# Kernel optimization log

Measured on AMD Instinct MI355X. Metric: run time of the kernel, lower is better.

Reference implementation:

```python
import jax, jax.numpy as jnp
import numpy as np

M, D, A, H = 16384, 256, 264, 8
HD = A // H  # 33
B = 512
THRESH = 0.1
DECAY = 0.95


def setup_inputs() -> dict:
    key = jax.random.key(0)
    ks = jax.random.split(key, 16)
    rn = lambda i, shape, scale=1.0: jax.random.normal(ks[i], shape, dtype=jnp.float32) * scale
    return {
        "features": rn(0, (B, D)),
        "gradients": rn(1, (B, D), 0.1),
        "mem_keys": rn(2, (M, D)),
        "mem_values": rn(3, (M, D)),
        "mem_ages": jax.random.uniform(ks[4], (M,), dtype=jnp.float32, minval=0.0, maxval=50.0),
        "mem_surprise": jax.random.uniform(ks[5], (M,), dtype=jnp.float32, minval=0.0, maxval=5.0),
        "Wk": rn(6, (D, D), 1.0 / np.sqrt(D)), "bk": jnp.zeros((D,), jnp.float32),
        "Wv": rn(7, (D, D), 1.0 / np.sqrt(D)), "bv": jnp.zeros((D,), jnp.float32),
        "Wp": rn(8, (D, A), 1.0 / np.sqrt(D)), "bp": jnp.zeros((A,), jnp.float32),
        "Win": rn(9, (A, 3 * A), 1.0 / np.sqrt(A)), "b_in": jnp.zeros((3 * A,), jnp.float32),
        "Wout": rn(10, (A, A), 1.0 / np.sqrt(A)), "bout": jnp.zeros((A,), jnp.float32),
        "Wo": rn(11, (A, D), 1.0 / np.sqrt(A)), "bo": jnp.zeros((D,), jnp.float32),
    }


def reference(features, gradients, mem_keys, mem_values, mem_ages, mem_surprise,
              Wk, bk, Wv, bv, Wp, bp, Win, b_in, Wout, bout, Wo, bo):
    # ---- compute_surprise: grad norm * min cdist to memory keys ----
    d2 = (jnp.sum(features * features, 1)[:, None]
          + jnp.sum(mem_keys * mem_keys, 1)[None, :]
          - 2.0 * features @ mem_keys.T)                      # [B, M]
    min_dist = jnp.sqrt(jnp.clip(jnp.min(d2, axis=1), 0.0))   # [B]
    surprise = jnp.linalg.norm(gradients, axis=-1) * min_dist  # [B]
    memorize = surprise > THRESH                               # [B] bool

    # ---- write_memory: sequential per-item eviction (argmin of decayed surprise) ----
    def step(carry, xs):
        mk, mv, ages, surp = carry
        feat, s_i, w = xs
        slot = jnp.argmin(surp * DECAY ** ages)
        mk = mk.at[slot].set(jnp.where(w, feat @ Wk + bk, mk[slot]))
        mv = mv.at[slot].set(jnp.where(w, feat @ Wv + bv, mv[slot]))
        ages = ages.at[slot].set(jnp.where(w, 0.0, ages[slot]))
        surp = surp.at[slot].set(jnp.where(w, s_i, surp[slot]))
        return (mk, mv, ages, surp), None

    (mem_keys, mem_values, mem_ages, mem_surprise), _ = jax.lax.scan(
        step, (mem_keys, mem_values, mem_ages, mem_surprise),
        (features, surprise, memorize))

    # ---- read_memory: project, 8-head cross attention (1 query vs M slots) ----
    q = features @ Wp + bp        # [B, A]
    kf = mem_keys @ Wp + bp       # [M, A]
    vf = mem_values @ Wp + bp     # [M, A]
    Wq_, Wk_, Wv_ = jnp.split(Win, 3, axis=1)
    bq_, bk_, bv_ = jnp.split(b_in, 3)
    qh = (q @ Wq_ + bq_).reshape(B, H, HD)
    kh = (kf @ Wk_ + bk_).reshape(M, H, HD)
    vh = (vf @ Wv_ + bv_).reshape(M, H, HD)
    scores = jnp.einsum('bhd,mhd->bhm', qh, kh) / np.float32(np.sqrt(HD))
    attn = jax.nn.softmax(scores, axis=-1)                    # [B, H, M]
    ctx = jnp.einsum('bhm,mhd->bhd', attn, vh).reshape(B, A)
    retrieved = (ctx @ Wout + bout) @ Wo + bo                 # [B, D]
    return retrieved
```

## Files before the change

kernel.cpp:

```cpp
#include <hip/hip_runtime.h>
#include <math.h>

typedef unsigned short ushort_t;
typedef float v4f __attribute__((ext_vector_type(4)));
typedef short v8s __attribute__((ext_vector_type(8)));

#define ATTN_MS 16

__device__ __forceinline__ unsigned fenc(float f){
  unsigned b = __float_as_uint(f);
  return (b & 0x80000000u) ? ~b : (b | 0x80000000u);
}
__device__ __forceinline__ float fdec(unsigned u){
  unsigned b = (u & 0x80000000u) ? (u ^ 0x80000000u) : ~u;
  return __uint_as_float(b);
}
__device__ __forceinline__ ushort_t bf16_rne(float x){
  unsigned u = __float_as_uint(x);
  unsigned r = u + 0x7FFFu + ((u >> 16) & 1u);
  return (ushort_t)(r >> 16);
}
__device__ __forceinline__ void split2(float x, ushort_t& h, ushort_t& l){
  unsigned u = __float_as_uint(x);
  unsigned r = u + 0x7FFFu + ((u >> 16) & 1u);
  h = (ushort_t)(r >> 16);
  float hf = __uint_as_float(r & 0xFFFF0000u);
  l = bf16_rne(x - hf);
}
__device__ __forceinline__ float bf2f(ushort_t x){ return __uint_as_float(((unsigned)x) << 16); }
union U8 { v8s v; ushort_t u[8]; };

__global__ __launch_bounds__(256) void prep_all(
    const float* __restrict__ features, const float* __restrict__ gradients,
    const float* __restrict__ mem_keys, const float* __restrict__ mem_values,
    ushort_t* __restrict__ FH, ushort_t* __restrict__ FL,
    ushort_t* __restrict__ MKH, ushort_t* __restrict__ MKL,
    ushort_t* __restrict__ MVH, ushort_t* __restrict__ MVL,
    float* __restrict__ k2, float* __restrict__ f2, float* __restrict__ gn,
    unsigned* __restrict__ minD2, ushort_t* __restrict__ VtGH, ushort_t* __restrict__ VtGL){
  int y = blockIdx.y, bx = blockIdx.x, t = threadIdx.x;
  if (y == 3){
    if (bx >= 3840) return;
    const int PER4 = 8*15*16384/4;
    int idx = bx*256 + t;
    if (idx >= 2*PER4) return;
    ushort_t* base = (idx < PER4) ? VtGH : VtGL;
    int i = (idx < PER4) ? idx : idx - PER4;
    int s = i*4;
    int hh = s / (15*16384);
    int r2 = s - hh*(15*16384);
    int row = 33 + (r2 >> 14);
    int col = r2 & 16383;
    ushort4 z; z.x = 0; z.y = 0; z.z = 0; z.w = 0;
    *(ushort4*)(base + (size_t)(hh*48 + row)*16384 + col) = z;
    return;
  }
  int wid = t >> 6, lane = t & 63;
  int row = bx*4 + wid;
  if (y == 2 && bx >= 128) return;
  const float* src = (y == 0) ? mem_keys : (y == 1) ? mem_values : features;
  float4 v = *(const float4*)(src + (size_t)row*256 + lane*4);
  ushort_t h0,h1,h2,h3,l0,l1,l2,l3;
  split2(v.x,h0,l0); split2(v.y,h1,l1); split2(v.z,h2,l2); split2(v.w,h3,l3);
  uint2 hp = make_uint2((unsigned)h0 | ((unsigned)h1<<16), (unsigned)h2 | ((unsigned)h3<<16));
  uint2 lp = make_uint2((unsigned)l0 | ((unsigned)l1<<16), (unsigned)l2 | ((unsigned)l3<<16));
  ushort_t* H = (y == 0) ? MKH : (y == 1) ? MVH : FH;
  ushort_t* L = (y == 0) ? MKL : (y == 1) ? MVL : FL;
  *(uint2*)(H + (size_t)row*256 + lane*4) = hp;
  *(uint2*)(L + (size_t)row*256 + lane*4) = lp;
  if (y == 1) return;
  float s = v.x*v.x + v.y*v.y + v.z*v.z + v.w*v.w;
  if (y == 0){
    for (int off = 32; off > 0; off >>= 1) s += __shfl_down(s, off, 64);
    if (lane == 0) k2[row] = s;
  } else {
    float4 g = *(const float4*)(gradients + (size_t)row*256 + lane*4);
    float tg = g.x*g.x + g.y*g.y + g.z*g.z + g.w*g.w;
    for (int off = 32; off > 0; off >>= 1){ s += __shfl_down(s, off, 64); tg += __shfl_down(tg, off, 64); }
    if (lane == 0){ f2[row] = s; gn[row] = sqrtf(tg); minD2[row] = 0xFFFFFFFFu; }
  }
}

__global__ __launch_bounds__(256) void gemm_bias(const float* __restrict__ A, const float* __restrict__ W,
                                                 const float* __restrict__ bias, float* __restrict__ C,
                                                 const float* __restrict__ W2, const float* __restrict__ bias2,
                                                 float* __restrict__ C2,
                                                 int M, int K, int N, int ldw, int woff){
  if (blockIdx.z == 1){ W = W2; bias = bias2; C = C2; }
  __shared__ float As[32*68];
  __shared__ float Ws[32*68];
  int m0 = blockIdx.x*64, c0 = blockIdx.y*64;
  int t = threadIdx.x;
  int mq = (t & 15)*4, cq = (t >> 4)*4;
  float acc[16];
  #pragma unroll
  for (int i = 0; i < 16; ++i) acc[i] = 0.f;
  for (int k0 = 0; k0 < K; k0 += 32){
    #pragma unroll
    for (int i = 0; i < 2; ++i){
      int idx = t + 256*i;
      int row = idx >> 3, kk = (idx & 7)*4;
      int gm = m0 + row, gk = k0 + kk;
      float x=0.f, y=0.f, z=0.f, w=0.f;
      if (gm < M){
        const float* ap = A + (size_t)gm*K + gk;
        if (gk + 3 < K){ float4 v = *(const float4*)ap; x=v.x; y=v.y; z=v.z; w=v.w; }
        else {
          if (gk   < K) x = ap[0];
          if (gk+1 < K) y = ap[1];
          if (gk+2 < K) z = ap[2];
          if (gk+3 < K) w = ap[3];
        }
      }
      As[(kk+0)*68+row]=x; As[(kk+1)*68+row]=y; As[(kk+2)*68+row]=z; As[(kk+3)*68+row]=w;
    }
    #pragma unroll
    for (int i = 0; i < 2; ++i){
      int idx = t + 256*i;
      int kk = idx >> 4, cc = (idx & 15)*4;
      int gk = k0 + kk, gc = c0 + cc;
      float4 v = make_float4(0.f,0.f,0.f,0.f);
      if (gk < K){
        const float* wp = W + (size_t)gk*ldw + woff + gc;
        if (gc + 3 < N) v = *(const float4*)wp;
        else {
          if (gc   < N) v.x = wp[0];
          if (gc+1 < N) v.y = wp[1];
          if (gc+2 < N) v.z = wp[2];
          if (gc+3 < N) v.w = wp[3];
        }
      }
      *(float4*)(Ws + kk*68 + cc) = v;
    }
    __syncthreads();
    #pragma unroll
    for (int j = 0; j < 32; ++j){
      float4 a = *(const float4*)(As + j*68 + mq);
      float4 w = *(const float4*)(Ws + j*68 + cq);
      acc[ 0]+=a.x*w.x; acc[ 1]+=a.x*w.y; acc[ 2]+=a.x*w.z; acc[ 3]+=a.x*w.w;
      acc[ 4]+=a.y*w.x; acc[ 5]+=a.y*w.y; acc[ 6]+=a.y*w.z; acc[ 7]+=a.y*w.w;
      acc[ 8]+=a.z*w.x; acc[ 9]+=a.z*w.y; acc[10]+=a.z*w.z; acc[11]+=a.z*w.w;
      acc[12]+=a.w*w.x; acc[13]+=a.w*w.y; acc[14]+=a.w*w.z; acc[15]+=a.w*w.w;
    }
    __syncthreads();
  }
  #pragma unroll
  for (int i = 0; i < 4; ++i){
    int gm = m0 + mq + i;
    if (gm >= M) continue;
    #pragma unroll
    for (int j = 0; j < 4; ++j){
      int gc = c0 + cq + j;
      if (gc >= N) continue;
      C[(size_t)gm*N + gc] = acc[i*4+j] + (bias ? bias[gc] : 0.f);
    }
  }
}

__global__ __launch_bounds__(256) void wprep_gemm(
    const float* __restrict__ Wp, const float* __restrict__ Win,
    const float* __restrict__ Wout, const float* __restrict__ Wo,
    const float* __restrict__ bp, const float* __restrict__ b_in,
    const float* __restrict__ bout, const float* __restrict__ bo,
    ushort_t* __restrict__ WtkH, ushort_t* __restrict__ WtkL,
    ushort_t* __restrict__ WtvH, ushort_t* __restrict__ WtvL,
    ushort_t* __restrict__ WtqH, ushort_t* __restrict__ WtqL,
    float* __restrict__ Wpk, float* __restrict__ Wpv, float* __restrict__ Wco,
    float* __restrict__ bpq, float* __restrict__ bpk, float* __restrict__ bpv, float* __restrict__ bco){
  __shared__ float As[32*68];
  __shared__ float Ws[32*68];
  int z = blockIdx.z;
  int t = threadIdx.x;
  if (z == 4){
    int flat = (blockIdx.x*5 + blockIdx.y)*256 + t;
    if (flat < 264){
      float a = b_in[flat];
      for (int k = 0; k < 264; ++k) a += bp[k]*Win[(size_t)k*792 + flat];
      bpq[flat] = a;
    } else if (flat < 528){
      int c = flat - 264;
      float a = b_in[264 + c];
      for (int k = 0; k < 264; ++k) a += bp[k]*Win[(size_t)k*792 + 264 + c];
      bpk[c] = a;
    } else if (flat < 792){
      int c = flat - 528;
      float a = b_in[528 + c];
      for (int k = 0; k < 264; ++k) a += bp[k]*Win[(size_t)k*792 + 528 + c];
      bpv[c] = a;
    } else if (flat < 1048){
      int c = flat - 792;
      float a = bo[c];
      for (int k = 0; k < 264; ++k) a += bout[k]*Wo[(size_t)k*256 + c];
      bco[c] = a;
    }
    return;
  }
  const float* A = (z < 3) ? Wp : Wout;
  const float* W = (z < 3) ? Win : Wo;
  const int M = (z < 3) ? 256 : 264;
  const int K = 264;
  const int N = (z < 3) ? 264 : 256;
  const int ldw = (z < 3) ? 792 : 256;
  const int woff = (z == 0) ? 264 : (z == 1) ? 528 : 0;
  int m0 = blockIdx.x*64, c0 = blockIdx.y*64;
  int mq = (t & 15)*4, cq = (t >> 4)*4;
  float acc[16];
  #pragma unroll
  for (int i = 0; i < 16; ++i) acc[i] = 0.f;
  for (int k0 = 0; k0 < K; k0 += 32){
    #pragma unroll
    for (int i = 0; i < 2; ++i){
      int idx = t + 256*i;
      int row = idx >> 3, kk = (idx & 7)*4;
      int gm = m0 + row, gk = k0 + kk;
      float x=0.f, y=0.f, z2=0.f, w=0.f;
      if (gm < M){
        const float* ap = A + (size_t)gm*K + gk;
        if (gk + 3 < K){ float4 v = *(const float4*)ap; x=v.x; y=v.y; z2=v.z; w=v.w; }
        else {
          if (gk   < K) x = ap[0];
          if (gk+1 < K) y = ap[1];
          if (gk+2 < K) z2 = ap[2];
          if (gk+3 < K) w = ap[3];
        }
      }
      As[(kk+0)*68+row]=x; As[(kk+1)*68+row]=y; As[(kk+2)*68+row]=z2; As[(kk+3)*68+row]=w;
    }
    #pragma unroll
    for (int i = 0; i < 2; ++i){
      int idx = t + 256*i;
      int kk = idx >> 4, cc = (idx & 15)*4;
      int gk = k0 + kk, gc = c0 + cc;
      float4 v = make_float4(0.f,0.f,0.f,0.f);
      if (gk < K){
        const float* wp = W + (size_t)gk*ldw + woff + gc;
        if (gc + 3 < N) v = *(const float4*)wp;
        else {
          if (gc   < N) v.x = wp[0];
          if (gc+1 < N) v.y = wp[1];
          if (gc+2 < N) v.z = wp[2];
          if (gc+3 < N) v.w = wp[3];
        }
      }
      *(float4*)(Ws + kk*68 + cc) = v;
    }
    __syncthreads();
    #pragma unroll
    for (int j = 0; j < 32; ++j){
      float4 a = *(const float4*)(As + j*68 + mq);
      float4 w = *(const float4*)(Ws + j*68 + cq);
      acc[ 0]+=a.x*w.x; acc[ 1]+=a.x*w.y; acc[ 2]+=a.x*w.z; acc[ 3]+=a.x*w.w;
      acc[ 4]+=a.y*w.x; acc[ 5]+=a.y*w.y; acc[ 6]+=a.y*w.z; acc[ 7]+=a.y*w.w;
      acc[ 8]+=a.z*w.x; acc[ 9]+=a.z*w.y; acc[10]+=a.z*w.z; acc[11]+=a.z*w.w;
      acc[12]+=a.w*w.x; acc[13]+=a.w*w.y; acc[14]+=a.w*w.z; acc[15]+=a.w*w.w;
    }
    __syncthreads();
  }
  if (z < 3){
    ushort_t* WH = (z==0) ? WtkH : (z==1) ? WtvH : WtqH;
    ushort_t* WL = (z==0) ? WtkL : (z==1) ? WtvL : WtqL;
    float* Wf = (z==0) ? Wpk : (z==1) ? Wpv : nullptr;
    #pragma unroll
    for (int i = 0; i < 4; ++i){
      int gm = m0 + mq + i;
      if (gm >= 256) continue;
      #pragma unroll
      for (int j = 0; j < 4; ++j){
        int gc = c0 + cq + j;
        float r = acc[i*4+j];
        ushort_t hh, ll; split2(r, hh, ll);
        WH[(size_t)gc*256 + gm] = hh;
        WL[(size_t)gc*256 + gm] = ll;
        if (Wf && gc < 264) Wf[(size_t)gm*264 + gc] = r;
      }
    }
  } else {
    #pragma unroll
    for (int i = 0; i < 4; ++i){
      int gm = m0 + mq + i;
      if (gm >= 264) continue;
      #pragma unroll
      for (int j = 0; j < 4; ++j){
        int gc = c0 + cq + j;
        if (gc < 256) Wco[(size_t)gm*256 + gc] = acc[i*4+j];
      }
    }
  }
}

__global__ __launch_bounds__(256) void big_mfma(
    const ushort_t* __restrict__ FH, const ushort_t* __restrict__ FL,
    const ushort_t* __restrict__ MKH, const ushort_t* __restrict__ MKL,
    const ushort_t* __restrict__ MVH, const ushort_t* __restrict__ MVL,
    const ushort_t* __restrict__ WtqH, const ushort_t* __restrict__ WtqL,
    const ushort_t* __restrict__ WtkH, const ushort_t* __restrict__ WtkL,
    const ushort_t* __restrict__ WtvH, const ushort_t* __restrict__ WtvL,
    const float* __restrict__ bpq, const float* __restrict__ bpk, const float* __restrict__ bpv,
    const float* __restrict__ k2,
    float* __restrict__ qh, ushort_t* __restrict__ khH, ushort_t* __restrict__ khL,
    ushort_t* __restrict__ VtGH, ushort_t* __restrict__ VtGL, unsigned* __restrict__ minD2){
  int z = blockIdx.z;
  int bx = blockIdx.x, by = blockIdx.y;
  if (z == 0 && bx >= 4) return;
  if (z != 3 && by >= 5) return;
  __shared__ ushort_t AsH[128*40];
  __shared__ ushort_t AsL[128*40];
  __shared__ ushort_t BsH[64*40];
  __shared__ ushort_t BsL[64*40];
  __shared__ unsigned sminU[64];
  const ushort_t* AH = (z == 0) ? FH : (z == 2) ? MVH : MKH;
  const ushort_t* AL = (z == 0) ? FL : (z == 2) ? MVL : MKL;
  const ushort_t* BH = (z == 0) ? WtqH : (z == 1) ? WtkH : (z == 2) ? WtvH : FH;
  const ushort_t* BL = (z == 0) ? WtqL : (z == 1) ? WtkL : WtvL;
  const float* bias = (z == 0) ? bpq : (z == 1) ? bpk : bpv;
  int t = threadIdx.x;
  int m0 = bx*128, n0 = by*64;
  int lane = t & 63, w = t >> 6;
  int wm = (w & 1)*64, wn = (w >> 1)*32;
  int l15 = lane & 15, q = lane >> 4;
  if (z == 3 && t < 64) sminU[t] = 0xFFFFFFFFu;
  v4f acc[4][2];
  #pragma unroll
  for (int i = 0; i < 4; ++i)
    #pragma unroll
    for (int j = 0; j < 2; ++j) acc[i][j] = (v4f){0.f,0.f,0.f,0.f};

  for (int k0 = 0; k0 < 256; k0 += 32){
    #pragma unroll
    for (int rdx = 0; rdx < 2; ++rdx){
      int idx = t + 256*rdx;
      int row = idx >> 2, ch = idx & 3;
      *(uint4*)(AsH + row*40 + ch*8) = *(const uint4*)(AH + (size_t)(m0+row)*256 + k0 + ch*8);
      if (z < 3)
        *(uint4*)(AsL + row*40 + ch*8) = *(const uint4*)(AL + (size_t)(m0+row)*256 + k0 + ch*8);
    }
    {
      int row = t >> 2, ch = t & 3;
      *(uint4*)(BsH + row*40 + ch*8) = *(const uint4*)(BH + (size_t)(n0+row)*256 + k0 + ch*8);
      if (z < 3)
        *(uint4*)(BsL + row*40 + ch*8) = *(const uint4*)(BL + (size_t)(n0+row)*256 + k0 + ch*8);
    }
    __syncthreads();
    if (z < 3){
      v8s aH[4], aL[4], bH[2], bL[2];
      #pragma unroll
      for (int im = 0; im < 4; ++im){
        aH[im] = *(const v8s*)(AsH + (wm + im*16 + l15)*40 + q*8);
        aL[im] = *(const v8s*)(AsL + (wm + im*16 + l15)*40 + q*8);
      }
      #pragma unroll
      for (int jn = 0; jn < 2; ++jn){
        bH[jn] = *(const v8s*)(BsH + (wn + jn*16 + l15)*40 + q*8);
        bL[jn] = *(const v8s*)(BsL + (wn + jn*16 + l15)*40 + q*8);
      }
      #pragma unroll
      for (int im = 0; im < 4; ++im)
        #pragma unroll
        for (int jn = 0; jn < 2; ++jn){
          acc[im][jn] = __builtin_amdgcn_mfma_f32_16x16x32_bf16(aH[im], bH[jn], acc[im][jn], 0, 0, 0);
          acc[im][jn] = __builtin_amdgcn_mfma_f32_16x16x32_bf16(aH[im], bL[jn], acc[im][jn], 0, 0, 0);
          acc[im][jn] = __builtin_amdgcn_mfma_f32_16x16x32_bf16(aL[im], bH[jn], acc[im][jn], 0, 0, 0);
        }
    } else {
      v8s aH[4], bH[2];
      #pragma unroll
      for (int im = 0; im < 4; ++im) aH[im] = *(const v8s*)(AsH + (wm + im*16 + l15)*40 + q*8);
      #pragma unroll
      for (int jn = 0; jn < 2; ++jn) bH[jn] = *(const v8s*)(BsH + (wn + jn*16 + l15)*40 + q*8);
      #pragma unroll
      for (int im = 0; im < 4; ++im)
        #pragma unroll
        for (int jn = 0; jn < 2; ++jn)
          acc[im][jn] = __builtin_amdgcn_mfma_f32_16x16x32_bf16(aH[im], bH[jn], acc[im][jn], 0, 0, 0);
    }
    __syncthreads();
  }

  if (z == 3){
    float kk[4][4];
    #pragma unroll
    for (int im = 0; im < 4; ++im)
      #pragma unroll
      for (int r = 0; r < 4; ++r) kk[im][r] = k2[m0 + wm + im*16 + q*4 + r];
    #pragma unroll
    for (int jn = 0; jn < 2; ++jn){
      float mv = INFINITY;
      #pragma unroll
      for (int im = 0; im < 4; ++im)
        #pragma unroll
        for (int r = 0; r < 4; ++r)
          mv = fminf(mv, kk[im][r] - 2.f*acc[im][jn][r]);
      mv = fminf(mv, __shfl_xor(mv, 16, 64));
      mv = fminf(mv, __shfl_xor(mv, 32, 64));
      if (q == 0) atomicMin(&sminU[wn + jn*16 + l15], fenc(mv));
    }
    __syncthreads();
    if (t < 64) atomicMin(&minD2[n0 + t], sminU[t]);
    return;
  }
  #pragma unroll
  for (int im = 0; im < 4; ++im){
    #pragma unroll
    for (int jn = 0; jn < 2; ++jn){
      int n = n0 + wn + jn*16 + l15;
      if (n >= 264) continue;
      float bv = bias[n];
      int mb = m0 + wm + im*16 + q*4;
      if (z == 0){
        #pragma unroll
        for (int r = 0; r < 4; ++r) qh[(size_t)(mb+r)*264 + n] = acc[im][jn][r] + bv;
      } else if (z == 1){
        int hh = n/33, dd = n - hh*33;
        int col = hh*40 + dd;
        #pragma unroll
        for (int r = 0; r < 4; ++r){
          ushort_t sh, sl; split2(acc[im][jn][r] + bv, sh, sl);
          khH[(size_t)(mb+r)*320 + col] = sh;
          khL[(size_t)(mb+r)*320 + col] = sl;
        }
      } else {
        int hh = n/33, dd = n - hh*33;
        size_t rowb = (size_t)(hh*48 + dd)*16384 + mb;
        ushort4 hv, lv;
        split2(acc[im][jn][0] + bv, hv.x, lv.x);
        split2(acc[im][jn][1] + bv, hv.y, lv.y);
        split2(acc[im][jn][2] + bv, hv.z, lv.z);
        split2(acc[im][jn][3] + bv, hv.w, lv.w);
        *(ushort4*)(VtGH + rowb) = hv;
        *(ushort4*)(VtGL + rowb) = lv;
      }
    }
  }
}

#define SCAN_CAP 1024
__global__ __launch_bounds__(1024) void scan_kernel(
    const float* __restrict__ mem_surprise, const float* __restrict__ mem_ages,
    const unsigned* __restrict__ minD2, const float* __restrict__ f2, const float* __restrict__ gn,
    float* __restrict__ parr, int* __restrict__ slotForB, int* __restrict__ lastB){
  __shared__ unsigned hist[2048];
  __shared__ float candV[SCAN_CAP];
  __shared__ int   candI[SCAN_CAP];
  __shared__ float tv[1024];
  __shared__ int   ti[1024];
  __shared__ float ssur[512];
  __shared__ int   smemz[512];
  __shared__ int   wtot[16];
  __shared__ int   sh_misc[8];
  int t = threadIdx.x;

  int mem = 0;
  if (t < 512){
    float d2 = fdec(minD2[t]) + f2[t];
    float s = gn[t]*sqrtf(fmaxf(d2, 0.f));
    ssur[t] = s;
    mem = (s > 0.1f) ? 1 : 0;
    smemz[t] = mem;
  }
  const float LN095 = -0.05129329438755058f;
  #pragma unroll
  for (int j = 0; j < 16; ++j){
    int m = t*16 + j;
    float p = mem_surprise[m] * __expf(mem_ages[m] * LN095);
    parr[m] = p;
    lastB[m] = -1;
  }
  hist[t] = 0u; hist[t + 1024] = 0u;
  if (t < 8) sh_misc[t] = (t == 3) ? 0x7F800000 : 0;
  __syncthreads();
  #pragma unroll
  for (int j = 0; j < 16; ++j){
    int m = t*16 + j;
    unsigned key = __float_as_uint(parr[m]) >> 20;
    if (key > 2047u) key = 2047u;
    atomicAdd(&hist[key], 1u);
  }
  __syncthreads();
  if (t < 512){ ti[t] = (int)(hist[4*t] + hist[4*t+1] + hist[4*t+2] + hist[4*t+3]); }
  __syncthreads();
  if (t < 32){ int s = 0; for (int i = 0; i < 16; ++i) s += ti[16*t + i]; ti[512 + t] = s; }
  __syncthreads();
  if (t == 0){
    int cum = 0, i2 = 0;
    for (; i2 < 32; ++i2){ if (cum + ti[512+i2] >= 512) break; cum += ti[512+i2]; }
    int i1 = i2*16;
    for (;; ++i1){ if (cum + ti[i1] >= 512) break; cum += ti[i1]; }
    int bin = i1*4;
    for (;; ++bin){ if (cum + (int)hist[bin] >= 512) break; cum += (int)hist[bin]; }
    sh_misc[1] = bin;
  }
  __syncthreads();
  int threshKey = sh_misc[1];
  #pragma unroll
  for (int j = 0; j < 16; ++j){
    int m = t*16 + j;
    unsigned key = __float_as_uint(parr[m]) >> 20;
    if (key > 2047u) key = 2047u;
    if ((int)key <= threshKey){
      int pos = atomicAdd(&sh_misc[0], 1);
      if (pos < SCAN_CAP){ candV[pos] = parr[m]; candI[pos] = m; }
    }
  }
  __syncthreads();
  int cnt = sh_misc[0];
  if (t >= cnt && t < SCAN_CAP){ candV[t] = INFINITY; candI[t] = 0x7FFFFFFF; }
  __syncthreads();
  for (int ksz = 2; ksz <= SCAN_CAP; ksz <<= 1){
    for (int jj = ksz >> 1; jj > 0; jj >>= 1){
      int ixj = t ^ jj;
      if (ixj > t){
        float v1 = candV[t], v2 = candV[ixj];
        int i1 = candI[t], i2 = candI[ixj];
        bool lt21 = (v2 < v1) || (v2 == v1 && i2 < i1);
        bool lt12 = (v1 < v2) || (v1 == v2 && i1 < i2);
        bool up = ((t & ksz) == 0);
        bool sw = up ? lt21 : lt12;
        if (sw){ candV[t] = v2; candI[t] = i2; candV[ixj] = v1; candI[ixj] = i1; }
      }
      __syncthreads();
    }
  }
  int lp = 0;
  if (t < 512){
    unsigned long long mask = __ballot(mem != 0);
    int lane = t & 63;
    lp = __popcll(mask & ((1ull << lane) - 1ull));
    if (lane == 0) wtot[t >> 6] = __popcll(mask);
  }
  if (t < 512 && mem) atomicMin(&sh_misc[3], __float_as_int(ssur[t]));
  __syncthreads();
  if (t == 0){
    int ksum = 0;
    for (int wv = 0; wv < 8; ++wv) ksum += wtot[wv];
    sh_misc[4] = ksum;
    bool okf = (cnt <= SCAN_CAP) && (ksum <= cnt);
    if (okf && ksum > 0){
      float minw = __int_as_float(sh_misc[3]);
      okf = (minw > candV[ksum - 1]);
    }
    sh_misc[2] = okf ? 1 : 0;
  }
  __syncthreads();
  if (sh_misc[2] == 1){
    if (t < 512){
      int wv = t >> 6, base = 0;
      for (int i = 0; i < wv; ++i) base += wtot[i];
      int slot = -1;
      if (mem){ slot = candI[base + lp]; atomicMax(&lastB[slot], t); }
      slotForB[t] = slot;
    }
  } else {
    for (int b = 0; b < 512; ++b){
      float bv = parr[t*16]; int bi = t*16;
      #pragma unroll
      for (int j = 1; j < 16; ++j){
        float v = parr[t*16 + j];
        if (v < bv){ bv = v; bi = t*16 + j; }
      }
      tv[t] = bv; ti[t] = bi;
      __syncthreads();
      for (int s = 512; s > 0; s >>= 1){
        if (t < s){
          float v2 = tv[t+s]; int i2 = ti[t+s];
          if (v2 < tv[t] || (v2 == tv[t] && i2 < ti[t])){ tv[t] = v2; ti[t] = i2; }
        }
        __syncthreads();
      }
      int slot = ti[0];
      int memb = smemz[b];
      if (t == 0) slotForB[b] = memb ? slot : -1;
      if (memb && t == (slot >> 4)) parr[slot] = ssur[b];
      __syncthreads();
    }
    if (t < 512){ int s = slotForB[t]; if (s >= 0) atomicMax(&lastB[s], t); }
  }
}

__global__ __launch_bounds__(64) void fixup_rows(const int* __restrict__ slotForB, const int* __restrict__ lastB,
                                                 const float* __restrict__ newK, const float* __restrict__ newV,
                                                 const float* __restrict__ Wpk, const float* __restrict__ Wpv,
                                                 const float* __restrict__ bpk, const float* __restrict__ bpv,
                                                 ushort_t* __restrict__ khH, ushort_t* __restrict__ khL,
                                                 ushort_t* __restrict__ VtH, ushort_t* __restrict__ VtL){
  int b = blockIdx.x;
  int slot = slotForB[b];
  if (slot < 0) return;
  if (lastB[slot] != b) return;
  __shared__ float kr[256], vr[256];
  int t = threadIdx.x;
  *(float4*)(kr + t*4) = *(const float4*)(newK + (size_t)b*256 + t*4);
  *(float4*)(vr + t*4) = *(const float4*)(newV + (size_t)b*256 + t*4);
  __syncthreads();
  for (int c = t; c < 264; c += 64){
    float aK = bpk[c], aV = bpv[c];
    for (int k = 0; k < 256; ++k){
      aK += kr[k]*Wpk[(size_t)k*264 + c];
      aV += vr[k]*Wpv[(size_t)k*264 + c];
    }
    int hh = c/33, dd = c - hh*33;
    ushort_t sh, sl;
    split2(aK, sh, sl);
    khH[(size_t)slot*320 + hh*40 + dd] = sh;
    khL[(size_t)slot*320 + hh*40 + dd] = sl;
    split2(aV, sh, sl);
    VtH[(size_t)(hh*48 + dd)*16384 + slot] = sh;
    VtL[(size_t)(hh*48 + dd)*16384 + slot] = sl;
  }
}

__global__ __launch_bounds__(256, 3) void attn_mfma(
    const float* __restrict__ qh, const ushort_t* __restrict__ khH, const ushort_t* __restrict__ khL,
    const ushort_t* __restrict__ VtGH, const ushort_t* __restrict__ VtGL,
    float* __restrict__ pm, float* __restrict__ pl, float* __restrict__ pctx){
  const int h = blockIdx.x, bt = blockIdx.y, ms = blockIdx.z;
  const int b0 = bt*64, mbase = ms*(16384/ATTN_MS);
  const int t = threadIdx.x, lane = t & 63, w = t >> 6;
  const int l15 = lane & 15, q = lane >> 4;
  __shared__ ushort_t KH[64*40], KL[64*40];
  __shared__ ushort_t VsH[48*72], VsL[48*72];
  __shared__ ushort_t PH[4*16*72], PL[4*16*72];
  __shared__ float k32f[64];
  const float scale = 0.17407765595569785f;

  const int bq = b0 + 16*w + l15;
  U8 qHU, qLU;
  {
    const float* qp = qh + (size_t)bq*264 + h*33 + q*8;
    #pragma unroll
    for (int j = 0; j < 8; ++j) split2(qp[j]*scale, qHU.u[j], qLU.u[j]);
  }
  const v8s bQH = qHU.v, bQL = qLU.v;
  const float q32v = qh[(size_t)bq*264 + h*33 + 32]*scale;
  float rMv = -INFINITY, rLv = 0.f;
  v4f cacc[3];
  #pragma unroll
  for (int i = 0; i < 3; ++i) cacc[i] = (v4f){0.f,0.f,0.f,0.f};
  ushort_t* PHw = PH + w*16*72;
  ushort_t* PLw = PL + w*16*72;

  for (int mt = 0; mt < 16384/ATTN_MS/64; ++mt){
    const int m0 = mbase + mt*64;
    __syncthreads();
    {
      int ml = t >> 2, ch = t & 3;
      *(uint4*)(KH + ml*40 + ch*8) = *(const uint4*)(khH + (size_t)(m0+ml)*320 + h*40 + ch*8);
      *(uint4*)(KL + ml*40 + ch*8) = *(const uint4*)(khL + (size_t)(m0+ml)*320 + h*40 + ch*8);
      if (t < 64)
        k32f[t] = bf2f(khH[(size_t)(m0+t)*320 + h*40 + 32]) + bf2f(khL[(size_t)(m0+t)*320 + h*40 + 32]);
    }
    #pragma unroll
    for (int i = 0; i < 3; ++i){
      int idx = t + 256*i;
      int arr = idx >= 384;
      int rem = idx - arr*384;
      int row = rem >> 3, ch = rem & 7;
      const ushort_t* g = (arr ? VtGL : VtGH) + (size_t)(h*48 + row)*16384 + m0 + ch*8;
      *(uint4*)((arr ? VsL : VsH) + row*72 + ch*8) = *(const uint4*)g;
    }
    __syncthreads();
    v4f s4[4];
    #pragma unroll
    for (int im = 0; im < 4; ++im){
      v8s aH = *(const v8s*)(KH + (im*16 + l15)*40 + q*8);
      v8s aL = *(const v8s*)(KL + (im*16 + l15)*40 + q*8);
      v4f sv = (v4f){0.f,0.f,0.f,0.f};
      sv = __builtin_amdgcn_mfma_f32_16x16x32_bf16(aH, bQH, sv, 0, 0, 0);
      sv = __builtin_amdgcn_mfma_f32_16x16x32_bf16(aH, bQL, sv, 0, 0, 0);
      sv = __builtin_amdgcn_mfma_f32_16x16x32_bf16(aL, bQH, sv, 0, 0, 0);
      s4[im] = sv;
    }
    #pragma unroll
    for (int im = 0; im < 4; ++im)
      #pragma unroll
      for (int r = 0; r < 4; ++r) s4[im][r] += k32f[im*16 + q*4 + r]*q32v;
    float mx = -INFINITY;
    #pragma unroll
    for (int im = 0; im < 4; ++im)
      #pragma unroll
      for (int r = 0; r < 4; ++r) mx = fmaxf(mx, s4[im][r]);
    mx = fmaxf(mx, __shfl_xor(mx, 16, 64));
    mx = fmaxf(mx, __shfl_xor(mx, 32, 64));
    float nm = fmaxf(rMv, mx);
    float alf = __expf(rMv - nm);
    rMv = nm;
    float sm = 0.f;
    #pragma unroll
    for (int im = 0; im < 4; ++im){
      v4f p;
      #pragma unroll
      for (int r = 0; r < 4; ++r){ p[r] = __expf(s4[im][r] - nm); sm += p[r]; }
      ushort4 hv, lv;
      split2(p[0], hv.x, lv.x); split2(p[1], hv.y, lv.y);
      split2(p[2], hv.z, lv.z); split2(p[3], hv.w, lv.w);
      *(ushort4*)(PHw + l15*72 + im*16 + q*4) = hv;
      *(ushort4*)(PLw + l15*72 + im*16 + q*4) = lv;
    }
    sm += __shfl_xor(sm, 16, 64);
    sm += __shfl_xor(sm, 32, 64);
    rLv = rLv*alf + sm;
    #pragma unroll
    for (int r = 0; r < 4; ++r){
      float ar = __shfl(alf, q*4 + r, 64);
      cacc[0][r] *= ar; cacc[1][r] *= ar; cacc[2][r] *= ar;
    }
    #pragma unroll
    for (int ks = 0; ks < 2; ++ks){
      v8s paH = *(const v8s*)(PHw + l15*72 + ks*32 + q*8);
      v8s paL = *(const v8s*)(PLw + l15*72 + ks*32 + q*8);
      #pragma unroll
      for (int tile = 0; tile < 3; ++tile){
        v8s vbH = *(const v8s*)(VsH + (tile*16 + l15)*72 + ks*32 + q*8);
        v8s vbL = *(const v8s*)(VsL + (tile*16 + l15)*72 + ks*32 + q*8);
        cacc[tile] = __builtin_amdgcn_mfma_f32_16x16x32_bf16(paH, vbH, cacc[tile], 0, 0, 0);
        cacc[tile] = __builtin_amdgcn_mfma_f32_16x16x32_bf16(paH, vbL, cacc[tile], 0, 0, 0);
        cacc[tile] = __builtin_amdgcn_mfma_f32_16x16x32_bf16(paL, vbH, cacc[tile], 0, 0, 0);
      }
    }
  }
  int g = (h*8 + bt)*ATTN_MS + ms;
  if (q == 0){
    pm[(size_t)g*64 + 16*w + l15] = rMv;
    pl[(size_t)g*64 + 16*w + l15] = rLv;
  }
  #pragma unroll
  for (int tile = 0; tile < 3; ++tile){
    int d = tile*16 + l15;
    if (d < 33){
      #pragma unroll
      for (int r = 0; r < 4; ++r)
        pctx[((size_t)g*64 + 16*w + q*4 + r)*33 + d] = cacc[tile][r];
    }
  }
}

__global__ __launch_bounds__(256) void combine_kernel(const float* __restrict__ pm, const float* __restrict__ pl,
                                                      const float* __restrict__ pctx, float* __restrict__ ctxf){
  int idx = blockIdx.x*256 + threadIdx.x;
  if (idx >= 512*264) return;
  int b = idx / 264, c = idx - b*264;
  int h = c / 33, d = c - h*33;
  int bt = b >> 6, bl = b & 63;
  int g0 = (h*8 + bt)*ATTN_MS;
  float gm = -INFINITY;
  for (int ms = 0; ms < ATTN_MS; ++ms) gm = fmaxf(gm, pm[(g0+ms)*64 + bl]);
  float L = 0.f, cv = 0.f;
  for (int ms = 0; ms < ATTN_MS; ++ms){
    int gg = (g0+ms)*64 + bl;
    float w = __expf(pm[gg] - gm);
    L += pl[gg]*w;
    cv += pctx[(size_t)gg*33 + d]*w;
  }
  ctxf[idx] = cv / L;
}

extern "C" void kernel_launch(void* const* d_in, const int* in_sizes, int n_in,
                              void* d_out, int out_size, void* d_ws, size_t ws_size,
                              hipStream_t stream){
  (void)in_sizes; (void)n_in; (void)out_size; (void)ws_size;
  const float* features     = (const float*)d_in[0];
  const float* gradients    = (const float*)d_in[1];
  const float* mem_keys     = (const float*)d_in[2];
  const float* mem_values   = (const float*)d_in[3];
  const float* mem_ages     = (const float*)d_in[4];
  const float* mem_surprise = (const float*)d_in[5];
  const float* Wk   = (const float*)d_in[6];
  const float* bk   = (const float*)d_in[7];
  const float* Wv   = (const float*)d_in[8];
  const float* bv   = (const float*)d_in[9];
  const float* Wp   = (const float*)d_in[10];
  const float* bp   = (const float*)d_in[11];
  const float* Win  = (const float*)d_in[12];
  const float* b_in = (const float*)d_in[13];
  const float* Wout = (const float*)d_in[14];
  const float* bout = (const float*)d_in[15];
  const float* Wo   = (const float*)d_in[16];
  const float* bo   = (const float*)d_in[17];
  float* out = (float*)d_out;

  float* w = (float*)d_ws;
  size_t off = 0;
  auto alloc = [&](size_t n)->float*{ float* p = w + off; off += (n + 63) & ~(size_t)63; return p; };
  float*    k2       = alloc(16384);
  unsigned* minD2    = (unsigned*)alloc(512);
  float*    f2       = alloc(512);
  float*    gn       = alloc(512);
  int*      slotForB = (int*)alloc(512);
  int*      lastB    = (int*)alloc(16384);
  float*    parr     = alloc(16384);
  float*    newK     = alloc((size_t)512*256);
  float*    newV     = alloc((size_t)512*256);
  float*    qh       = alloc((size_t)512*264);
  ushort_t* khH      = (ushort_t*)alloc((size_t)16384*320/2);
  ushort_t* khL      = (ushort_t*)alloc((size_t)16384*320/2);
  ushort_t* VtGH     = (ushort_t*)alloc((size_t)8*48*16384/2);
  ushort_t* VtGL     = (ushort_t*)alloc((size_t)8*48*16384/2);
  float*    MKbase   = alloc((size_t)16384*256/2*2);
  ushort_t* MKH      = (ushort_t*)MKbase;
  ushort_t* MKL      = (ushort_t*)(MKbase + (size_t)16384*256/2);
  float*    MVbase   = alloc((size_t)16384*256/2*2);
  ushort_t* MVH      = (ushort_t*)MVbase;
  ushort_t* MVL      = (ushort_t*)(MVbase + (size_t)16384*256/2);
  ushort_t* FH       = (ushort_t*)alloc((size_t)512*256/2);
  ushort_t* FL       = (ushort_t*)alloc((size_t)512*256/2);
  float*    Wpk      = alloc((size_t)256*264);
  float*    Wpv      = alloc((size_t)256*264);
  float*    Wco      = alloc((size_t)264*256);
  ushort_t* WtkH     = (ushort_t*)alloc((size_t)320*256/2);
  ushort_t* WtkL     = (ushort_t*)alloc((size_t)320*256/2);
  ushort_t* WtvH     = (ushort_t*)alloc((size_t)320*256/2);
  ushort_t* WtvL     = (ushort_t*)alloc((size_t)320*256/2);
  ushort_t* WtqH     = (ushort_t*)alloc((size_t)320*256/2);
  ushort_t* WtqL     = (ushort_t*)alloc((size_t)320*256/2);
  float*    bpq      = alloc(264);
  float*    bpk      = alloc(264);
  float*    bpv      = alloc(264);
  float*    bco      = alloc(256);
  float*    pm       = MKbase;
  float*    pl       = MKbase + (size_t)ATTN_MS*64*64;
  float*    ctxf     = pl + (size_t)ATTN_MS*64*64;
  float*    pctx     = MVbase;

  prep_all<<<dim3(4096,4), 256, 0, stream>>>(features, gradients, mem_keys, mem_values,
      FH, FL, MKH, MKL, MVH, MVL, k2, f2, gn, minD2, VtGH, VtGL);

  wprep_gemm<<<dim3(5,5,5), 256, 0, stream>>>(Wp, Win, Wout, Wo, bp, b_in, bout, bo,
      WtkH, WtkL, WtvH, WtvL, WtqH, WtqL, Wpk, Wpv, Wco, bpq, bpk, bpv, bco);

  gemm_bias<<<dim3(8,4,2), 256, 0, stream>>>(features, Wk, bk, newK, Wv, bv, newV, 512, 256, 256, 256, 0);

  big_mfma<<<dim3(128,8,4), 256, 0, stream>>>(FH, FL, MKH, MKL, MVH, MVL,
      WtqH, WtqL, WtkH, WtkL, WtvH, WtvL, bpq, bpk, bpv, k2,
      qh, khH, khL, VtGH, VtGL, minD2);

  scan_kernel<<<1, 1024, 0, stream>>>(mem_surprise, mem_ages, minD2, f2, gn, parr, slotForB, lastB);
  fixup_rows<<<512, 64, 0, stream>>>(slotForB, lastB, newK, newV, Wpk, Wpv, bpk, bpv, khH, khL, VtGH, VtGL);

  attn_mfma<<<dim3(8,8,ATTN_MS), 256, 0, stream>>>(qh, khH, khL, VtGH, VtGL, pm, pl, pctx);
  combine_kernel<<<528, 256, 0, stream>>>(pm, pl, pctx, ctxf);
  gemm_bias<<<dim3(8,4,1), 256, 0, stream>>>(ctxf, Wco, bco, out, Wco, bco, out, 512, 264, 256, 256, 0);
}
```

Before: 427.8 us.

## Stage GEMM and attention tiles via direct global-to-LDS loads with XOR swizzle

Replaces register-staged global-to-shared copies in big_mfma and attn_mfma with global_load_lds 16-byte direct transfers. Padded LDS rows are removed, and the V tile gets an XOR swizzle to avoid bank conflicts. Occupancy hints rise to 4 blocks per CU. The aim is to cut VGPR pressure and load/store instruction overhead. The trade-off is that the unpadded K/A tiles may now hit LDS bank conflicts.

```diff
diff --git a/kernel.cpp b/kernel.cpp
--- a/kernel.cpp
+++ b/kernel.cpp
@@ -1,5 +1,6 @@
 #include <hip/hip_runtime.h>
 #include <math.h>
+#include <stdint.h>
 
 typedef unsigned short ushort_t;
 typedef float v4f __attribute__((ext_vector_type(4)));
@@ -29,6 +30,13 @@
 }
 __device__ __forceinline__ float bf2f(ushort_t x){ return __uint_as_float(((unsigned)x) << 16); }
 union U8 { v8s v; ushort_t u[8]; };
+
+__device__ __forceinline__ void gl2lds16(const void* g, void* l){
+  __builtin_amdgcn_global_load_lds(
+      (const __attribute__((address_space(1))) unsigned int*)(uintptr_t)g,
+      (__attribute__((address_space(3))) unsigned int*)(unsigned int)(uintptr_t)l,
+      16, 0, 0);
+}
 
 __global__ __launch_bounds__(256) void prep_all(
     const float* __restrict__ features, const float* __restrict__ gradients,
@@ -288,7 +296,7 @@
   }
 }
 
-__global__ __launch_bounds__(256) void big_mfma(
+__global__ __launch_bounds__(256, 4) void big_mfma(
     const ushort_t* __restrict__ FH, const ushort_t* __restrict__ FL,
     const ushort_t* __restrict__ MKH, const ushort_t* __restrict__ MKL,
     const ushort_t* __restrict__ MVH, const ushort_t* __restrict__ MVL,
@@ -303,10 +311,10 @@
   int bx = blockIdx.x, by = blockIdx.y;
   if (z == 0 && bx >= 4) return;
   if (z != 3 && by >= 5) return;
-  __shared__ ushort_t AsH[128*40];
-  __shared__ ushort_t AsL[128*40];
-  __shared__ ushort_t BsH[64*40];
-  __shared__ ushort_t BsL[64*40];
+  __shared__ ushort_t AsH[128*32];
+  __shared__ ushort_t AsL[128*32];
+  __shared__ ushort_t BsH[64*32];
+  __shared__ ushort_t BsL[64*32];
   __shared__ unsigned sminU[64];
   const ushort_t* AH = (z == 0) ? FH : (z == 2) ? MVH : MKH;
   const ushort_t* AL = (z == 0) ? FL : (z == 2) ? MVL : MKL;
@@ -327,31 +335,31 @@
 
   for (int k0 = 0; k0 < 256; k0 += 32){
     #pragma unroll
-    for (int rdx = 0; rdx < 2; ++rdx){
-      int idx = t + 256*rdx;
-      int row = idx >> 2, ch = idx & 3;
-      *(uint4*)(AsH + row*40 + ch*8) = *(const uint4*)(AH + (size_t)(m0+row)*256 + k0 + ch*8);
-      if (z < 3)
-        *(uint4*)(AsL + row*40 + ch*8) = *(const uint4*)(AL + (size_t)(m0+row)*256 + k0 + ch*8);
+    for (int c = 0; c < 2; ++c){
+      int u0 = (c*4 + w)*64;
+      int u  = u0 + lane;
+      int row = u >> 2, ch = u & 3;
+      gl2lds16(AH + (size_t)(m0+row)*256 + k0 + ch*8, AsH + (size_t)u0*8);
+      if (z < 3) gl2lds16(AL + (size_t)(m0+row)*256 + k0 + ch*8, AsL + (size_t)u0*8);
     }
     {
-      int row = t >> 2, ch = t & 3;
-      *(uint4*)(BsH + row*40 + ch*8) = *(const uint4*)(BH + (size_t)(n0+row)*256 + k0 + ch*8);
-      if (z < 3)
-        *(uint4*)(BsL + row*40 + ch*8) = *(const uint4*)(BL + (size_t)(n0+row)*256 + k0 + ch*8);
+      int u = w*64 + lane;
+      int row = u >> 2, ch = u & 3;
+      gl2lds16(BH + (size_t)(n0+row)*256 + k0 + ch*8, BsH + (size_t)w*512);
+      if (z < 3) gl2lds16(BL + (size_t)(n0+row)*256 + k0 + ch*8, BsL + (size_t)w*512);
     }
     __syncthreads();
     if (z < 3){
       v8s aH[4], aL[4], bH[2], bL[2];
       #pragma unroll
       for (int im = 0; im < 4; ++im){
-        aH[im] = *(const v8s*)(AsH + (wm + im*16 + l15)*40 + q*8);
-        aL[im] = *(const v8s*)(AsL + (wm + im*16 + l15)*40 + q*8);
+        aH[im] = *(const v8s*)(AsH + (wm + im*16 + l15)*32 + q*8);
+        aL[im] = *(const v8s*)(AsL + (wm + im*16 + l15)*32 + q*8);
       }
       #pragma unroll
       for (int jn = 0; jn < 2; ++jn){
-        bH[jn] = *(const v8s*)(BsH + (wn + jn*16 + l15)*40 + q*8);
-        bL[jn] = *(const v8s*)(BsL + (wn + jn*16 + l15)*40 + q*8);
+        bH[jn] = *(const v8s*)(BsH + (wn + jn*16 + l15)*32 + q*8);
+        bL[jn] = *(const v8s*)(BsL + (wn + jn*16 + l15)*32 + q*8);
       }
       #pragma unroll
       for (int im = 0; im < 4; ++im)
@@ -364,9 +372,9 @@
     } else {
       v8s aH[4], bH[2];
       #pragma unroll
-      for (int im = 0; im < 4; ++im) aH[im] = *(const v8s*)(AsH + (wm + im*16 + l15)*40 + q*8);
-      #pragma unroll
-      for (int jn = 0; jn < 2; ++jn) bH[jn] = *(const v8s*)(BsH + (wn + jn*16 + l15)*40 + q*8);
+      for (int im = 0; im < 4; ++im) aH[im] = *(const v8s*)(AsH + (wm + im*16 + l15)*32 + q*8);
+      #pragma unroll
+      for (int jn = 0; jn < 2; ++jn) bH[jn] = *(const v8s*)(BsH + (wn + jn*16 + l15)*32 + q*8);
       #pragma unroll
       for (int im = 0; im < 4; ++im)
         #pragma unroll
@@ -608,7 +616,7 @@
   }
 }
 
-__global__ __launch_bounds__(256, 3) void attn_mfma(
+__global__ __launch_bounds__(256, 4) void attn_mfma(
     const float* __restrict__ qh, const ushort_t* __restrict__ khH, const ushort_t* __restrict__ khL,
     const ushort_t* __restrict__ VtGH, const ushort_t* __restrict__ VtGL,
     float* __restrict__ pm, float* __restrict__ pl, float* __restrict__ pctx){
@@ -616,8 +624,8 @@
   const int b0 = bt*64, mbase = ms*(16384/ATTN_MS);
   const int t = threadIdx.x, lane = t & 63, w = t >> 6;
   const int l15 = lane & 15, q = lane >> 4;
-  __shared__ ushort_t KH[64*40], KL[64*40];
-  __shared__ ushort_t VsH[48*72], VsL[48*72];
+  __shared__ ushort_t KH[64*32], KL[64*32];
+  __shared__ ushort_t VsH[48*64], VsL[48*64];
   __shared__ ushort_t PH[4*16*72], PL[4*16*72];
   __shared__ float k32f[64];
   const float scale = 0.17407765595569785f;
@@ -642,27 +650,31 @@
     const int m0 = mbase + mt*64;
     __syncthreads();
     {
-      int ml = t >> 2, ch = t & 3;
-      *(uint4*)(KH + ml*40 + ch*8) = *(const uint4*)(khH + (size_t)(m0+ml)*320 + h*40 + ch*8);
-      *(uint4*)(KL + ml*40 + ch*8) = *(const uint4*)(khL + (size_t)(m0+ml)*320 + h*40 + ch*8);
-      if (t < 64)
-        k32f[t] = bf2f(khH[(size_t)(m0+t)*320 + h*40 + 32]) + bf2f(khL[(size_t)(m0+t)*320 + h*40 + 32]);
-    }
-    #pragma unroll
-    for (int i = 0; i < 3; ++i){
-      int idx = t + 256*i;
-      int arr = idx >= 384;
-      int rem = idx - arr*384;
-      int row = rem >> 3, ch = rem & 7;
-      const ushort_t* g = (arr ? VtGL : VtGH) + (size_t)(h*48 + row)*16384 + m0 + ch*8;
-      *(uint4*)((arr ? VsL : VsH) + row*72 + ch*8) = *(const uint4*)g;
+      int u = w*64 + lane;
+      int row = u >> 2, ch = u & 3;
+      gl2lds16(khH + (size_t)(m0+row)*320 + h*40 + ch*8, KH + (size_t)w*512);
+      gl2lds16(khL + (size_t)(m0+row)*320 + h*40 + ch*8, KL + (size_t)w*512);
+    }
+    if (t < 64)
+      k32f[t] = bf2f(khH[(size_t)(m0+t)*320 + h*40 + 32]) + bf2f(khL[(size_t)(m0+t)*320 + h*40 + 32]);
+    #pragma unroll
+    for (int c = 0; c < 2; ++c){
+      if (c == 0 || w < 2){
+        int u0 = c*256 + w*64;
+        int u = u0 + lane;
+        int dd = u >> 3, chl = u & 7;
+        int gch = chl ^ (dd & 7);
+        size_t gi = (size_t)(h*48 + dd)*16384 + m0 + gch*8;
+        gl2lds16(VtGH + gi, VsH + (size_t)u0*8);
+        gl2lds16(VtGL + gi, VsL + (size_t)u0*8);
+      }
     }
     __syncthreads();
     v4f s4[4];
     #pragma unroll
     for (int im = 0; im < 4; ++im){
-      v8s aH = *(const v8s*)(KH + (im*16 + l15)*40 + q*8);
-      v8s aL = *(const v8s*)(KL + (im*16 + l15)*40 + q*8);
+      v8s aH = *(const v8s*)(KH + (im*16 + l15)*32 + q*8);
+      v8s aL = *(const v8s*)(KL + (im*16 + l15)*32 + q*8);
       v4f sv = (v4f){0.f,0.f,0.f,0.f};
       sv = __builtin_amdgcn_mfma_f32_16x16x32_bf16(aH, bQH, sv, 0, 0, 0);
       sv = __builtin_amdgcn_mfma_f32_16x16x32_bf16(aH, bQL, sv, 0, 0, 0);
@@ -709,8 +721,10 @@
       v8s paL = *(const v8s*)(PLw + l15*72 + ks*32 + q*8);
       #pragma unroll
       for (int tile = 0; tile < 3; ++tile){
-        v8s vbH = *(const v8s*)(VsH + (tile*16 + l15)*72 + ks*32 + q*8);
-        v8s vbL = *(const v8s*)(VsL + (tile*16 + l15)*72 + ks*32 + q*8);
+        int vrow = tile*16 + l15;
+        int mch = (ks*4 + q) ^ (l15 & 7);
+        v8s vbH = *(const v8s*)(VsH + vrow*64 + mch*8);
+        v8s vbL = *(const v8s*)(VsL + vrow*64 + mch*8);
         cacc[tile] = __builtin_amdgcn_mfma_f32_16x16x32_bf16(paH, vbH, cacc[tile], 0, 0, 0);
         cacc[tile] = __builtin_amdgcn_mfma_f32_16x16x32_bf16(paH, vbL, cacc[tile], 0, 0, 0);
         cacc[tile] = __builtin_amdgcn_mfma_f32_16x16x32_bf16(paL, vbH, cacc[tile], 0, 0, 0);
```

Result: faster. 398.8 us (-6.8%).
